# Optimization experiments

Measured on AMD Instinct MI355X. Metric: run time of the kernel, lower is better.

## Reference

```python
import jax, jax.numpy as jnp
import numpy as np

B, S, D_MODEL = 4, 2048, 1024
H, DK, DV = 16, 64, 64
MASKED = False


def setup_inputs() -> dict:
    key = jax.random.key(0)
    ks = jax.random.split(key, 7)
    return {
        "q": jax.random.normal(ks[0], (B, S, D_MODEL), dtype=jnp.float32),
        "k": jax.random.normal(ks[1], (B, S, D_MODEL), dtype=jnp.float32),
        "v": jax.random.normal(ks[2], (B, S, D_MODEL), dtype=jnp.float32),
        "Wq": jax.random.normal(ks[3], (H, D_MODEL, DK), dtype=jnp.float32) * 0.05,
        "Wk": jax.random.normal(ks[4], (H, D_MODEL, DK), dtype=jnp.float32) * 0.05,
        "Wv": jax.random.normal(ks[5], (H, D_MODEL, DV), dtype=jnp.float32) * 0.05,
        "Wo": jax.random.normal(ks[6], (H * DV, D_MODEL), dtype=jnp.float32) * 0.05,
    }


def reference(q, k, v, Wq, Wk, Wv, Wo):
    # Per-head projections, batched over heads instead of a Python loop.
    Q = jnp.einsum("bsd,hdk->bhsk", q, Wq)  # [B,H,S,Dk]
    K = jnp.einsum("btd,hdk->bhtk", k, Wk)  # [B,H,S,Dk]
    V = jnp.einsum("btd,hdv->bhtv", v, Wv)  # [B,H,S,Dv]

    scale = 1.0 / jnp.sqrt(jnp.asarray(DK, dtype=Q.dtype))
    scores = jnp.einsum("bhsk,bhtk->bhst", Q, K) * scale  # [B,H,S,S]
    if MASKED:
        causal = jnp.tril(jnp.ones((S, S), dtype=bool))
        scores = jnp.where(causal, scores, jnp.finfo(scores.dtype).min)
    attn = jax.nn.softmax(scores, axis=-1)
    heads = jnp.einsum("bhst,bhtv->bhsv", attn, V)  # [B,H,S,Dv]

    # concat heads along feature dim (tf.concat(heads, axis=-1)) then Wo projection
    multi = heads.transpose(0, 2, 1, 3).reshape(q.shape[0], q.shape[1], H * DV)
    return multi @ Wo  # [B,S,D_MODEL]
```

## Files before the change

### kernel.cpp

```cpp
#include <hip/hip_runtime.h>
#include <hip/hip_bf16.h>

typedef __attribute__((ext_vector_type(8))) short short8;
typedef __attribute__((ext_vector_type(4))) short short4v;
typedef __attribute__((ext_vector_type(4))) float f32x4;
typedef __attribute__((ext_vector_type(16))) float f32x16;
typedef __attribute__((ext_vector_type(2))) float f32x2;
typedef __attribute__((ext_vector_type(4))) unsigned short us4;
typedef __attribute__((ext_vector_type(2))) unsigned int u32x2;
typedef __attribute__((ext_vector_type(4))) unsigned int u32x4;

#define NB 4
#define SEQ 2048
#define DMODEL 1024
#define NH 16
#define DHEAD 64
#define QSCALE 0.18033688011112042f
#define FM 34.0f

static __device__ __forceinline__ unsigned short f2bf(float f) {
    __hip_bfloat16 h = __float2bfloat16(f);
    return *reinterpret_cast<unsigned short*>(&h);
}
static __device__ __forceinline__ unsigned int cvt_pk(float lo, float hi) {
    float2 t; t.x = lo; t.y = hi;
    __hip_bfloat162 h = __float22bfloat162_rn(t);
    return *reinterpret_cast<unsigned int*>(&h);
}

typedef __attribute__((address_space(3))) unsigned int lds_u32_t;
typedef __attribute__((address_space(1))) const unsigned int glob_u32_t;
static __device__ __forceinline__ void gl_lds16(const unsigned short* g, unsigned short* l) {
    __builtin_amdgcn_global_load_lds((glob_u32_t*)g, (lds_u32_t*)l, 16, 0, 0);
}

static __device__ __forceinline__ void pl32swap(unsigned& a, unsigned& b) {
    asm("v_permlane32_swap_b32 %0, %1" : "+v"(a), "+v"(b));
}

__global__ __launch_bounds__(256) void prep_x(const float* __restrict__ q,
                                              const float* __restrict__ k,
                                              const float* __restrict__ v,
                                              unsigned short* __restrict__ xq,
                                              unsigned short* __restrict__ xk,
                                              unsigned short* __restrict__ xv) {
    const int z = blockIdx.y;
    int i = blockIdx.x * 256 + threadIdx.x;
    const float* in = z == 0 ? q : (z == 1 ? k : v);
    unsigned short* out = z == 0 ? xq : (z == 1 ? xk : xv);
    f32x4 val = ((const f32x4*)in)[i];
    u32x2 o;
    o.x = cvt_pk(val.x, val.y);
    o.y = cvt_pk(val.z, val.w);
    ((u32x2*)out)[i] = o;
}

__global__ __launch_bounds__(256) void prep_w(const float* __restrict__ wq,
                                              const float* __restrict__ wk,
                                              const float* __restrict__ wv,
                                              const float* __restrict__ wo,
                                              unsigned short* __restrict__ oq,
                                              unsigned short* __restrict__ ok,
                                              unsigned short* __restrict__ ov,
                                              unsigned short* __restrict__ oo) {
    __shared__ unsigned short T[64 * 65];
    const int z = blockIdx.y;
    const int tid = threadIdx.x;
    const int ty = tid >> 4, tx = tid & 15;
    const float* in;
    unsigned short* out;
    size_t ibase, obase;
    int instride;
    float scale = 1.0f;
    if (z < 3) {
        in = z == 0 ? wq : (z == 1 ? wk : wv);
        out = z == 0 ? oq : (z == 1 ? ok : ov);
        if (z == 0) scale = QSCALE;
        const int h = blockIdx.x >> 4, dt = blockIdx.x & 15;
        ibase = (size_t)(h * 1024 + dt * 64) * 64;
        instride = 64;
        obase = (size_t)h * 64 * 1024 + dt * 64;
    } else {
        in = wo;
        out = oo;
        const int rt = blockIdx.x >> 4, ct = blockIdx.x & 15;
        ibase = (size_t)(rt * 64) * 1024 + ct * 64;
        instride = 1024;
        obase = (size_t)(ct * 64) * 1024 + rt * 64;
    }
#pragma unroll
    for (int p = 0; p < 4; p++) {
        const int row = p * 16 + ty;
        f32x4 v = *(const f32x4*)&in[ibase + (size_t)row * instride + tx * 4];
#pragma unroll
        for (int j = 0; j < 4; j++) T[(tx * 4 + j) * 65 + row] = f2bf(v[j] * scale);
    }
    __syncthreads();
#pragma unroll
    for (int qq = 0; qq < 4; qq++) {
        const int orow = qq * 16 + ty;
        us4 o;
#pragma unroll
        for (int j = 0; j < 4; j++) o[j] = T[orow * 65 + tx * 4 + j];
        *(us4*)&out[obase + (size_t)orow * 1024 + tx * 4] = o;
    }
}

struct GemmAcc { f32x4 a[4][4]; };

static __device__ __forceinline__ void gemm_core(const unsigned short* __restrict__ A,
                                                 const unsigned short* __restrict__ Bt,
                                                 unsigned short (*As)[4096],
                                                 unsigned short (*Bs)[4096],
                                                 int m0, int n0, int K, GemmAcc& acc) {
    const int tid = threadIdx.x;
    const int w = tid >> 6, l = tid & 63;
    const int lane16 = l & 15, quad = l >> 4;
    const int wr = w >> 1, wc = w & 1;

#pragma unroll
    for (int a = 0; a < 4; a++)
#pragma unroll
        for (int b = 0; b < 4; b++) acc.a[a][b] = (f32x4){0.f, 0.f, 0.f, 0.f};

    const int i0 = 2 * w, i1 = 2 * w + 1;
    const int rs = l >> 2;
    const int cc = ((l & 3) ^ ((l >> 3) & 3)) * 8;
    const unsigned short* a0 = A + (size_t)(m0 + i0 * 16 + rs) * K + cc;
    const unsigned short* a1 = A + (size_t)(m0 + i1 * 16 + rs) * K + cc;
    const unsigned short* b0 = Bt + (size_t)(n0 + i0 * 16 + rs) * K + cc;
    const unsigned short* b1 = Bt + (size_t)(n0 + i1 * 16 + rs) * K + cc;

    const int cl = (quad ^ ((lane16 >> 1) & 3)) * 8;
    const int ra = (wr * 64 + lane16) * 32 + cl;
    const int rb = (wc * 64 + lane16) * 32 + cl;

    for (int k0 = 0; k0 < K; k0 += 64) {
        __syncthreads();
#pragma unroll
        for (int h = 0; h < 2; h++) {
            gl_lds16(a0 + k0 + h * 32, &As[h][i0 * 512]);
            gl_lds16(a1 + k0 + h * 32, &As[h][i1 * 512]);
            gl_lds16(b0 + k0 + h * 32, &Bs[h][i0 * 512]);
            gl_lds16(b1 + k0 + h * 32, &Bs[h][i1 * 512]);
        }
        __syncthreads();
#pragma unroll
        for (int h = 0; h < 2; h++) {
            short8 af[4], bf[4];
#pragma unroll
            for (int mt = 0; mt < 4; mt++) af[mt] = *(const short8*)&As[h][ra + mt * 512];
#pragma unroll
            for (int nt = 0; nt < 4; nt++) bf[nt] = *(const short8*)&Bs[h][rb + nt * 512];
#pragma unroll
            for (int mt = 0; mt < 4; mt++)
#pragma unroll
                for (int nt = 0; nt < 4; nt++)
                    acc.a[mt][nt] = __builtin_amdgcn_mfma_f32_16x16x32_bf16(
                        af[mt], bf[nt], acc.a[mt][nt], 0, 0, 0);
        }
    }
}

__global__ __launch_bounds__(256) void gemm_qkv(const unsigned short* __restrict__ xq,
                                                const unsigned short* __restrict__ xk,
                                                const unsigned short* __restrict__ xv,
                                                const unsigned short* __restrict__ wq,
                                                const unsigned short* __restrict__ wk,
                                                const unsigned short* __restrict__ wv,
                                                unsigned short* __restrict__ Qb,
                                                unsigned short* __restrict__ Kb,
                                                unsigned short* __restrict__ Vtb) {
    __shared__ unsigned short As[2][4096];
    __shared__ unsigned short Bs[2][4096];
    const int z = blockIdx.z;
    const unsigned short* A = z == 0 ? xq : (z == 1 ? xk : xv);
    const unsigned short* Bt = z == 0 ? wq : (z == 1 ? wk : wv);
    unsigned short* out = z == 0 ? Qb : (z == 1 ? Kb : Vtb);

    const int m0 = blockIdx.x * 128, n0 = blockIdx.y * 128;
    GemmAcc acc;
    gemm_core(A, Bt, As, Bs, m0, n0, DMODEL, acc);

    const int l = threadIdx.x & 63, w = threadIdx.x >> 6;
    const int lane16 = l & 15, quad = l >> 4;
    const int wr = w >> 1, wc = w & 1;
    if (z < 2) {
#pragma unroll
        for (int mt = 0; mt < 4; mt++)
#pragma unroll
            for (int nt = 0; nt < 4; nt++)
#pragma unroll
                for (int r = 0; r < 4; r++) {
                    int m = m0 + wr * 64 + mt * 16 + quad * 4 + r;
                    int n = n0 + wc * 64 + nt * 16 + lane16;
                    int b_ = m >> 11, s = m & 2047, h = n >> 6, kk = n & 63;
                    out[((size_t)((b_ * NH + h) * SEQ + s) << 6) + kk] = f2bf(acc.a[mt][nt][r]);
                }
    } else {
#pragma unroll
        for (int mt = 0; mt < 4; mt++)
#pragma unroll
            for (int nt = 0; nt < 4; nt++) {
                int m = m0 + wr * 64 + mt * 16 + quad * 4;
                int n = n0 + wc * 64 + nt * 16 + lane16;
                int b_ = m >> 11, s = m & 2047, h = n >> 6, kk = n & 63;
                u32x2 pk;
                pk.x = cvt_pk(acc.a[mt][nt][0], acc.a[mt][nt][1]);
                pk.y = cvt_pk(acc.a[mt][nt][2], acc.a[mt][nt][3]);
                *(u32x2*)&out[(size_t)((b_ * NH + h) * DHEAD + kk) * SEQ + s] = pk;
            }
    }
}

__global__ __launch_bounds__(256) void gemm_out(const unsigned short* __restrict__ A,
                                                const unsigned short* __restrict__ Bt,
                                                float* __restrict__ C) {
    __shared__ unsigned short As[2][4096];
    __shared__ unsigned short Bs[2][4096];
    const int m0 = blockIdx.x * 128, n0 = blockIdx.y * 128;
    GemmAcc acc;
    gemm_core(A, Bt, As, Bs, m0, n0, DMODEL, acc);

    const int l = threadIdx.x & 63, w = threadIdx.x >> 6;
    const int lane16 = l & 15, quad = l >> 4;
    const int wr = w >> 1, wc = w & 1;
#pragma unroll
    for (int mt = 0; mt < 4; mt++)
#pragma unroll
        for (int nt = 0; nt < 4; nt++)
#pragma unroll
            for (int r = 0; r < 4; r++) {
                int m = m0 + wr * 64 + mt * 16 + quad * 4 + r;
                int n = n0 + wc * 64 + nt * 16 + lane16;
                C[(size_t)m * DMODEL + n] = acc.a[mt][nt][r];
            }
}

__global__ __launch_bounds__(256) void flash_attn(const unsigned short* __restrict__ Q,
                                                  const unsigned short* __restrict__ Kg,
                                                  const unsigned short* __restrict__ Vt,
                                                  unsigned short* __restrict__ Hout) {
    __shared__ unsigned short Ks[2][4096];
    __shared__ unsigned short Vs[2][4096];

    const int tid = threadIdx.x;
    const int w = tid >> 6, l = tid & 63;
    const int l31 = l & 31, hi = l >> 5;
    const int wg = ((blockIdx.x & 7) << 7) | (blockIdx.x >> 3);
    const int bh = wg >> 4, b_ = bh >> 4, h = bh & 15;
    const int s0 = (wg & 15) * 128;

    const unsigned short* Qbh = Q + (size_t)bh * SEQ * DHEAD;
    const unsigned short* Kbh = Kg + (size_t)bh * SEQ * DHEAD;
    const unsigned short* Vbh = Vt + (size_t)bh * DHEAD * SEQ;

    short8 qf[4];
    {
        const unsigned short* qp = Qbh + (size_t)(s0 + w * 32 + l31) * DHEAD + hi * 8;
#pragma unroll
        for (int dk = 0; dk < 4; dk++) qf[dk] = *(const short8*)(qp + dk * 16);
    }

    f32x16 o0, o1, scinit;
#pragma unroll
    for (int r = 0; r < 16; r++) { o0[r] = 0.f; o1[r] = 0.f; scinit[r] = -FM; }
    f32x2 lsum2 = (f32x2){0.f, 0.f};

    int offs[4];
#pragma unroll
    for (int i = 0; i < 4; i++) offs[i] = l31 * 64 + ((((i << 1) + hi) ^ (l31 & 7)) << 3);

    const int i0 = 2 * w, i1 = 2 * w + 1;
    const int rs = l >> 3;
    const int cgs = ((l & 7) ^ rs) * 8;
    const unsigned short* kg0 = Kbh + (size_t)(i0 * 8 + rs) * DHEAD + cgs;
    const unsigned short* kg1 = Kbh + (size_t)(i1 * 8 + rs) * DHEAD + cgs;
    const unsigned short* vg0 = Vbh + (size_t)(i0 * 8 + rs) * SEQ + cgs;
    const unsigned short* vg1 = Vbh + (size_t)(i1 * 8 + rs) * SEQ + cgs;

#define STAGE(B, T)                                            \
    do {                                                       \
        const size_t ko_ = (size_t)(T) * (64 * DHEAD);         \
        const int vo_ = (T) * 64;                              \
        gl_lds16(kg0 + ko_, &Ks[B][i0 * 512]);                 \
        gl_lds16(kg1 + ko_, &Ks[B][i1 * 512]);                 \
        gl_lds16(vg0 + vo_, &Vs[B][i0 * 512]);                 \
        gl_lds16(vg1 + vo_, &Vs[B][i1 * 512]);                 \
    } while (0)

    auto compute = [&](const unsigned short* kb, const unsigned short* vb) {
#pragma unroll
        for (int tc = 0; tc < 2; tc++) {
            short8 kf0 = *(const short8*)(kb + tc * 2048 + offs[0]);
            short8 kf1 = *(const short8*)(kb + tc * 2048 + offs[1]);
            short8 kf2 = *(const short8*)(kb + tc * 2048 + offs[2]);
            short8 kf3 = *(const short8*)(kb + tc * 2048 + offs[3]);
            f32x16 sc = __builtin_amdgcn_mfma_f32_32x32x16_bf16(kf0, qf[0], scinit, 0, 0, 0);
            sc = __builtin_amdgcn_mfma_f32_32x32x16_bf16(kf1, qf[1], sc, 0, 0, 0);
            sc = __builtin_amdgcn_mfma_f32_32x32x16_bf16(kf2, qf[2], sc, 0, 0, 0);
            sc = __builtin_amdgcn_mfma_f32_32x32x16_bf16(kf3, qf[3], sc, 0, 0, 0);
            float p[16];
#pragma unroll
            for (int r = 0; r < 16; r++) p[r] = __builtin_amdgcn_exp2f(sc[r]);
#pragma unroll
            for (int r = 0; r < 16; r += 2) {
                f32x2 t; t.x = p[r]; t.y = p[r + 1];
                lsum2 += t;
            }
#pragma unroll
            for (int ntp = 0; ntp < 2; ntp++) {
                const int nt = tc * 2 + ntp;
                unsigned c0 = cvt_pk(p[8 * ntp + 0], p[8 * ntp + 1]);
                unsigned c1 = cvt_pk(p[8 * ntp + 2], p[8 * ntp + 3]);
                unsigned c2 = cvt_pk(p[8 * ntp + 4], p[8 * ntp + 5]);
                unsigned c3 = cvt_pk(p[8 * ntp + 6], p[8 * ntp + 7]);
                pl32swap(c0, c2);
                pl32swap(c1, c3);
                u32x4 pk4;
                pk4.x = c0; pk4.y = c1; pk4.z = c2; pk4.w = c3;
                const short8 pbv = __builtin_bit_cast(short8, pk4);
                short8 vf0 = *(const short8*)(vb + offs[nt]);
                short8 vf1 = *(const short8*)(vb + 2048 + offs[nt]);
                o0 = __builtin_amdgcn_mfma_f32_32x32x16_bf16(vf0, pbv, o0, 0, 0, 0);
                o1 = __builtin_amdgcn_mfma_f32_32x32x16_bf16(vf1, pbv, o1, 0, 0, 0);
            }
        }
    };

    STAGE(0, 0);
    asm volatile("s_waitcnt vmcnt(0)" ::: "memory");
    __builtin_amdgcn_s_barrier();

    const int NT = SEQ / 64;
    for (int t = 0; t < NT; t += 2) {
        STAGE(1, t + 1);
        asm volatile("" ::: "memory");
        compute(Ks[0], Vs[0]);
        asm volatile("" ::: "memory");
        asm volatile("s_waitcnt vmcnt(0)" ::: "memory");
        __builtin_amdgcn_s_barrier();

        if (t + 2 < NT) STAGE(0, t + 2);
        asm volatile("" ::: "memory");
        compute(Ks[1], Vs[1]);
        asm volatile("" ::: "memory");
        asm volatile("s_waitcnt vmcnt(0)" ::: "memory");
        __builtin_amdgcn_s_barrier();
    }
#undef STAGE

    float lsv = lsum2.x + lsum2.y;
    lsv += __shfl_xor(lsv, 32);
    const float inv = 1.f / lsv;
    const int s = s0 + w * 32 + l31;
    unsigned short* hp = Hout + (size_t)(b_ * SEQ + s) * DMODEL + h * 64 + hi * 4;
#pragma unroll
    for (int g = 0; g < 4; g++) {
        u32x2 ov;
        ov.x = cvt_pk(o0[4 * g + 0] * inv, o0[4 * g + 1] * inv);
        ov.y = cvt_pk(o0[4 * g + 2] * inv, o0[4 * g + 3] * inv);
        *(u32x2*)(hp + g * 8) = ov;
        ov.x = cvt_pk(o1[4 * g + 0] * inv, o1[4 * g + 1] * inv);
        ov.y = cvt_pk(o1[4 * g + 2] * inv, o1[4 * g + 3] * inv);
        *(u32x2*)(hp + 32 + g * 8) = ov;
    }
}

extern "C" void kernel_launch(void* const* d_in, const int* in_sizes, int n_in,
                              void* d_out, int out_size, void* d_ws, size_t ws_size,
                              hipStream_t stream) {
    const float* q  = (const float*)d_in[0];
    const float* k  = (const float*)d_in[1];
    const float* v  = (const float*)d_in[2];
    const float* Wq = (const float*)d_in[3];
    const float* Wk = (const float*)d_in[4];
    const float* Wv = (const float*)d_in[5];
    const float* Wo = (const float*)d_in[6];

    const size_t SZ_X = (size_t)NB * SEQ * DMODEL * 2;
    const size_t SZ_W = (size_t)DMODEL * DMODEL * 2;
    char* ws = (char*)d_ws;
    unsigned short* xq  = (unsigned short*)(ws);
    unsigned short* xk  = (unsigned short*)(ws + SZ_X);
    unsigned short* xv  = (unsigned short*)(ws + 2 * SZ_X);
    unsigned short* wqt = (unsigned short*)(ws + 3 * SZ_X);
    unsigned short* wkt = (unsigned short*)(ws + 3 * SZ_X + SZ_W);
    unsigned short* wvt = (unsigned short*)(ws + 3 * SZ_X + 2 * SZ_W);
    unsigned short* wot = (unsigned short*)(ws + 3 * SZ_X + 3 * SZ_W);
    unsigned short* Qb  = (unsigned short*)(ws + 3 * SZ_X + 4 * SZ_W);
    unsigned short* Kb  = (unsigned short*)(ws + 4 * SZ_X + 4 * SZ_W);
    unsigned short* Vtb = (unsigned short*)(ws + 5 * SZ_X + 4 * SZ_W);
    unsigned short* hd  = (unsigned short*)(ws + 6 * SZ_X + 4 * SZ_W);
    if (ws_size < 7 * SZ_X + 4 * SZ_W) return;

    const int n4 = NB * SEQ * DMODEL / 4;
    prep_x<<<dim3(n4 / 256, 3), 256, 0, stream>>>(q, k, v, xq, xk, xv);
    prep_w<<<dim3(256, 4), 256, 0, stream>>>(Wq, Wk, Wv, Wo, wqt, wkt, wvt, wot);

    const int M = NB * SEQ;
    gemm_qkv<<<dim3(M / 128, DMODEL / 128, 3), 256, 0, stream>>>(
        xq, xk, xv, wqt, wkt, wvt, Qb, Kb, Vtb);

    flash_attn<<<dim3((SEQ / 128) * NB * NH), 256, 0, stream>>>(Qb, Kb, Vtb, hd);

    gemm_out<<<dim3(M / 128, DMODEL / 128), 256, 0, stream>>>(hd, wot, (float*)d_out);
}
```

Measured before the change: 336.9 us.

## Replace 128x128 GEMMs with 256x256 tiles and a 4-stage prefetched LDS pipeline

Measured after the change: 343.1 us. About the same (+1.8%).

```diff
diff --git a/kernel.cpp b/kernel.cpp
--- a/kernel.cpp
+++ b/kernel.cpp
@@ -106,134 +106,160 @@
     }
 }
 
-struct GemmAcc { f32x4 a[4][4]; };
-
-static __device__ __forceinline__ void gemm_core(const unsigned short* __restrict__ A,
-                                                 const unsigned short* __restrict__ Bt,
-                                                 unsigned short (*As)[4096],
-                                                 unsigned short (*Bs)[4096],
-                                                 int m0, int n0, int K, GemmAcc& acc) {
+static __device__ __forceinline__ void gemm256_core(const unsigned short* __restrict__ A,
+                                                    const unsigned short* __restrict__ Bt,
+                                                    unsigned short* AsL, unsigned short* BsL,
+                                                    int m0, int n0, f32x4 (&acc)[8][4]) {
     const int tid = threadIdx.x;
     const int w = tid >> 6, l = tid & 63;
     const int lane16 = l & 15, quad = l >> 4;
-    const int wr = w >> 1, wc = w & 1;
-
-#pragma unroll
-    for (int a = 0; a < 4; a++)
-#pragma unroll
-        for (int b = 0; b < 4; b++) acc.a[a][b] = (f32x4){0.f, 0.f, 0.f, 0.f};
-
-    const int i0 = 2 * w, i1 = 2 * w + 1;
+    const int wr = w >> 2, wc = w & 3;
+
+#pragma unroll
+    for (int mt = 0; mt < 8; mt++)
+#pragma unroll
+        for (int nt = 0; nt < 4; nt++) acc[mt][nt] = (f32x4){0.f, 0.f, 0.f, 0.f};
+
     const int rs = l >> 2;
     const int cc = ((l & 3) ^ ((l >> 3) & 3)) * 8;
-    const unsigned short* a0 = A + (size_t)(m0 + i0 * 16 + rs) * K + cc;
-    const unsigned short* a1 = A + (size_t)(m0 + i1 * 16 + rs) * K + cc;
-    const unsigned short* b0 = Bt + (size_t)(n0 + i0 * 16 + rs) * K + cc;
-    const unsigned short* b1 = Bt + (size_t)(n0 + i1 * 16 + rs) * K + cc;
+    const unsigned short* aP0 = A + (size_t)(m0 + (2 * w + 0) * 16 + rs) * DMODEL + cc;
+    const unsigned short* aP1 = A + (size_t)(m0 + (2 * w + 1) * 16 + rs) * DMODEL + cc;
+    const unsigned short* bP0 = Bt + (size_t)(n0 + (2 * w + 0) * 16 + rs) * DMODEL + cc;
+    const unsigned short* bP1 = Bt + (size_t)(n0 + (2 * w + 1) * 16 + rs) * DMODEL + cc;
 
     const int cl = (quad ^ ((lane16 >> 1) & 3)) * 8;
-    const int ra = (wr * 64 + lane16) * 32 + cl;
-    const int rb = (wc * 64 + lane16) * 32 + cl;
-
-    for (int k0 = 0; k0 < K; k0 += 64) {
-        __syncthreads();
-#pragma unroll
-        for (int h = 0; h < 2; h++) {
-            gl_lds16(a0 + k0 + h * 32, &As[h][i0 * 512]);
-            gl_lds16(a1 + k0 + h * 32, &As[h][i1 * 512]);
-            gl_lds16(b0 + k0 + h * 32, &Bs[h][i0 * 512]);
-            gl_lds16(b1 + k0 + h * 32, &Bs[h][i1 * 512]);
-        }
-        __syncthreads();
-#pragma unroll
-        for (int h = 0; h < 2; h++) {
-            short8 af[4], bf[4];
-#pragma unroll
-            for (int mt = 0; mt < 4; mt++) af[mt] = *(const short8*)&As[h][ra + mt * 512];
-#pragma unroll
-            for (int nt = 0; nt < 4; nt++) bf[nt] = *(const short8*)&Bs[h][rb + nt * 512];
-#pragma unroll
-            for (int mt = 0; mt < 4; mt++)
-#pragma unroll
-                for (int nt = 0; nt < 4; nt++)
-                    acc.a[mt][nt] = __builtin_amdgcn_mfma_f32_16x16x32_bf16(
-                        af[mt], bf[nt], acc.a[mt][nt], 0, 0, 0);
-        }
-    }
-}
-
-__global__ __launch_bounds__(256) void gemm_qkv(const unsigned short* __restrict__ xq,
-                                                const unsigned short* __restrict__ xk,
-                                                const unsigned short* __restrict__ xv,
-                                                const unsigned short* __restrict__ wq,
-                                                const unsigned short* __restrict__ wk,
-                                                const unsigned short* __restrict__ wv,
-                                                unsigned short* __restrict__ Qb,
-                                                unsigned short* __restrict__ Kb,
-                                                unsigned short* __restrict__ Vtb) {
-    __shared__ unsigned short As[2][4096];
-    __shared__ unsigned short Bs[2][4096];
+    const int rf = lane16 * 32 + cl;
+
+#define SA(KT) do { unsigned short* d_ = AsL + ((KT) & 3) * 8192;            \
+        gl_lds16(aP0 + (KT) * 32, d_ + (2 * w + 0) * 512);                   \
+        gl_lds16(aP1 + (KT) * 32, d_ + (2 * w + 1) * 512); } while (0)
+#define SB(KT) do { unsigned short* d_ = BsL + ((KT) & 3) * 8192;            \
+        gl_lds16(bP0 + (KT) * 32, d_ + (2 * w + 0) * 512);                   \
+        gl_lds16(bP1 + (KT) * 32, d_ + (2 * w + 1) * 512); } while (0)
+
+    SA(0); SB(0); SA(1); SB(1);
+
+    for (int kt = 0; kt < 32; ++kt) {
+        if (kt < 31) { asm volatile("s_waitcnt vmcnt(4)" ::: "memory"); }
+        else         { asm volatile("s_waitcnt vmcnt(0)" ::: "memory"); }
+        __builtin_amdgcn_s_barrier();
+        asm volatile("" ::: "memory");
+        const unsigned short* as = AsL + (kt & 3) * 8192;
+        const unsigned short* bs = BsL + (kt & 3) * 8192;
+        short8 bf[4], af[4];
+#pragma unroll
+        for (int nt = 0; nt < 4; nt++) bf[nt] = *(const short8*)&bs[(wc * 4 + nt) * 512 + rf];
+#pragma unroll
+        for (int mt = 0; mt < 4; mt++) af[mt] = *(const short8*)&as[(wr * 8 + mt) * 512 + rf];
+        if (kt < 30) SA(kt + 2);
+        __builtin_amdgcn_s_barrier();
+        asm volatile("s_waitcnt lgkmcnt(0)" ::: "memory");
+        __builtin_amdgcn_s_setprio(1);
+#pragma unroll
+        for (int mt = 0; mt < 4; mt++)
+#pragma unroll
+            for (int nt = 0; nt < 4; nt++)
+                acc[mt][nt] = __builtin_amdgcn_mfma_f32_16x16x32_bf16(af[mt], bf[nt],
+                                                                      acc[mt][nt], 0, 0, 0);
+        __builtin_amdgcn_s_setprio(0);
+        __builtin_amdgcn_s_barrier();
+        asm volatile("" ::: "memory");
+#pragma unroll
+        for (int mt = 0; mt < 4; mt++) af[mt] = *(const short8*)&as[(wr * 8 + 4 + mt) * 512 + rf];
+        if (kt < 30) SB(kt + 2);
+        __builtin_amdgcn_s_barrier();
+        asm volatile("s_waitcnt lgkmcnt(0)" ::: "memory");
+        __builtin_amdgcn_s_setprio(1);
+#pragma unroll
+        for (int mt = 0; mt < 4; mt++)
+#pragma unroll
+            for (int nt = 0; nt < 4; nt++)
+                acc[4 + mt][nt] = __builtin_amdgcn_mfma_f32_16x16x32_bf16(af[mt], bf[nt],
+                                                                          acc[4 + mt][nt], 0, 0, 0);
+        __builtin_amdgcn_s_setprio(0);
+    }
+#undef SA
+#undef SB
+}
+
+static __device__ __forceinline__ int xcd_m0_256(int bx) {
+    return (((bx & 7) << 2) | (bx >> 3)) * 256;
+}
+
+__global__ __launch_bounds__(512, 2) void gemm_qkv256(const unsigned short* __restrict__ xq,
+                                                      const unsigned short* __restrict__ xk,
+                                                      const unsigned short* __restrict__ xv,
+                                                      const unsigned short* __restrict__ wq,
+                                                      const unsigned short* __restrict__ wk,
+                                                      const unsigned short* __restrict__ wv,
+                                                      unsigned short* __restrict__ Qb,
+                                                      unsigned short* __restrict__ Kb,
+                                                      unsigned short* __restrict__ Vtb) {
+    extern __shared__ unsigned short smem[];
+    unsigned short* AsL = smem;
+    unsigned short* BsL = smem + 32768;
     const int z = blockIdx.z;
     const unsigned short* A = z == 0 ? xq : (z == 1 ? xk : xv);
     const unsigned short* Bt = z == 0 ? wq : (z == 1 ? wk : wv);
     unsigned short* out = z == 0 ? Qb : (z == 1 ? Kb : Vtb);
 
-    const int m0 = blockIdx.x * 128, n0 = blockIdx.y * 128;
-    GemmAcc acc;
-    gemm_core(A, Bt, As, Bs, m0, n0, DMODEL, acc);
+    const int m0 = xcd_m0_256(blockIdx.x), n0 = blockIdx.y * 256;
+    f32x4 acc[8][4];
+    gemm256_core(A, Bt, AsL, BsL, m0, n0, acc);
 
     const int l = threadIdx.x & 63, w = threadIdx.x >> 6;
     const int lane16 = l & 15, quad = l >> 4;
-    const int wr = w >> 1, wc = w & 1;
+    const int wr = w >> 2, wc = w & 3;
     if (z < 2) {
 #pragma unroll
-        for (int mt = 0; mt < 4; mt++)
+        for (int mt = 0; mt < 8; mt++)
 #pragma unroll
             for (int nt = 0; nt < 4; nt++)
 #pragma unroll
                 for (int r = 0; r < 4; r++) {
-                    int m = m0 + wr * 64 + mt * 16 + quad * 4 + r;
+                    int m = m0 + wr * 128 + mt * 16 + quad * 4 + r;
                     int n = n0 + wc * 64 + nt * 16 + lane16;
                     int b_ = m >> 11, s = m & 2047, h = n >> 6, kk = n & 63;
-                    out[((size_t)((b_ * NH + h) * SEQ + s) << 6) + kk] = f2bf(acc.a[mt][nt][r]);
+                    out[((size_t)((b_ * NH + h) * SEQ + s) << 6) + kk] = f2bf(acc[mt][nt][r]);
                 }
     } else {
 #pragma unroll
-        for (int mt = 0; mt < 4; mt++)
+        for (int mt = 0; mt < 8; mt++)
 #pragma unroll
             for (int nt = 0; nt < 4; nt++) {
-                int m = m0 + wr * 64 + mt * 16 + quad * 4;
+                int m = m0 + wr * 128 + mt * 16 + quad * 4;
                 int n = n0 + wc * 64 + nt * 16 + lane16;
                 int b_ = m >> 11, s = m & 2047, h = n >> 6, kk = n & 63;
                 u32x2 pk;
-                pk.x = cvt_pk(acc.a[mt][nt][0], acc.a[mt][nt][1]);
-                pk.y = cvt_pk(acc.a[mt][nt][2], acc.a[mt][nt][3]);
+                pk.x = cvt_pk(acc[mt][nt][0], acc[mt][nt][1]);
+                pk.y = cvt_pk(acc[mt][nt][2], acc[mt][nt][3]);
                 *(u32x2*)&out[(size_t)((b_ * NH + h) * DHEAD + kk) * SEQ + s] = pk;
             }
     }
 }
 
-__global__ __launch_bounds__(256) void gemm_out(const unsigned short* __restrict__ A,
-                                                const unsigned short* __restrict__ Bt,
-                                                float* __restrict__ C) {
-    __shared__ unsigned short As[2][4096];
-    __shared__ unsigned short Bs[2][4096];
-    const int m0 = blockIdx.x * 128, n0 = blockIdx.y * 128;
-    GemmAcc acc;
-    gemm_core(A, Bt, As, Bs, m0, n0, DMODEL, acc);
+__global__ __launch_bounds__(512, 2) void gemm_out256(const unsigned short* __restrict__ A,
+                                                      const unsigned short* __restrict__ Bt,
+                                                      float* __restrict__ C) {
+    extern __shared__ unsigned short smem[];
+    unsigned short* AsL = smem;
+    unsigned short* BsL = smem + 32768;
+    const int m0 = xcd_m0_256(blockIdx.x), n0 = blockIdx.y * 256;
+    f32x4 acc[8][4];
+    gemm256_core(A, Bt, AsL, BsL, m0, n0, acc);
 
     const int l = threadIdx.x & 63, w = threadIdx.x >> 6;
     const int lane16 = l & 15, quad = l >> 4;
-    const int wr = w >> 1, wc = w & 1;
-#pragma unroll
-    for (int mt = 0; mt < 4; mt++)
+    const int wr = w >> 2, wc = w & 3;
+#pragma unroll
+    for (int mt = 0; mt < 8; mt++)
 #pragma unroll
         for (int nt = 0; nt < 4; nt++)
 #pragma unroll
             for (int r = 0; r < 4; r++) {
-                int m = m0 + wr * 64 + mt * 16 + quad * 4 + r;
+                int m = m0 + wr * 128 + mt * 16 + quad * 4 + r;
                 int n = n0 + wc * 64 + nt * 16 + lane16;
-                C[(size_t)m * DMODEL + n] = acc.a[mt][nt][r];
+                C[(size_t)m * DMODEL + n] = acc[mt][nt][r];
             }
 }
 
@@ -394,15 +420,23 @@
     unsigned short* hd  = (unsigned short*)(ws + 6 * SZ_X + 4 * SZ_W);
     if (ws_size < 7 * SZ_X + 4 * SZ_W) return;
 
+    static int attr_done = 0;
+    if (!attr_done) {
+        hipFuncSetAttribute((const void*)gemm_qkv256,
+                            hipFuncAttributeMaxDynamicSharedMemorySize, 131072);
+        hipFuncSetAttribute((const void*)gemm_out256,
+                            hipFuncAttributeMaxDynamicSharedMemorySize, 131072);
+        attr_done = 1;
+    }
+
     const int n4 = NB * SEQ * DMODEL / 4;
     prep_x<<<dim3(n4 / 256, 3), 256, 0, stream>>>(q, k, v, xq, xk, xv);
     prep_w<<<dim3(256, 4), 256, 0, stream>>>(Wq, Wk, Wv, Wo, wqt, wkt, wvt, wot);
 
-    const int M = NB * SEQ;
-    gemm_qkv<<<dim3(M / 128, DMODEL / 128, 3), 256, 0, stream>>>(
+    gemm_qkv256<<<dim3(32, 4, 3), 512, 131072, stream>>>(
         xq, xk, xv, wqt, wkt, wvt, Qb, Kb, Vtb);
 
     flash_attn<<<dim3((SEQ / 128) * NB * NH), 256, 0, stream>>>(Qb, Kb, Vtb, hd);
 
-    gemm_out<<<dim3(M / 128, DMODEL / 128), 256, 0, stream>>>(hd, wot, (float*)d_out);
-}
+    gemm_out256<<<dim3(32, 4), 512, 131072, stream>>>(hd, wot, (float*)d_out);
+}
```
